# Performance work log

Measured on AMD Instinct MI355X. Metric: run time of the kernel, lower is better.

Reference implementation:

```python
import jax, jax.numpy as jnp
import numpy as np
from jax.scipy.special import erf

B, N, D = 4, 4096, 2
MU, ALPHA, BETA, SIGMA = 1.0, 0.8, 2.0, 0.02


def setup_inputs() -> dict:
    key = jax.random.key(0)
    k1, k2 = jax.random.split(key)
    locations = jax.random.uniform(k1, (B, N, D), dtype=jnp.float32)  # events in unit box
    times = jnp.sort(jax.random.uniform(k2, (B, N), dtype=jnp.float32), axis=-1)  # sorted event times
    # ragged sequence lengths via mask
    lengths = jnp.array([N, N - 256, N - 512, N - 1024], dtype=jnp.int32)
    mask = jnp.arange(N)[None, :] < lengths[:, None]
    return {
        "locations": locations,
        "times": times,
        "mask": mask,
        "mu": jnp.float32(MU),
        "alpha": jnp.float32(ALPHA),
        "beta": jnp.float32(BETA),
        "sigma": jnp.float32(SIGMA),
        "spatial_low": jnp.zeros((D,), jnp.float32),
        "spatial_high": jnp.ones((D,), jnp.float32),
        "t_end": jnp.float32(1.0),
    }


def reference(locations, times, mask, mu, alpha, beta, sigma, spatial_low, spatial_high, t_end):
    """Hawkes log_prob: sum_i log lambda*(s_i, t_i | H_{t_i}) - Lambda(D x [0, T])."""
    d = locations.shape[-1]
    # --- intensity at each event given its (strictly earlier, masked) history ---
    dt = times[:, :, None] - times[:, None, :]            # [B,N,N] t_i - t_j
    valid = (dt > 0.0) & mask[:, None, :]                 # causal + observed history
    dt_safe = jnp.where(valid, dt, 0.0)
    diff = locations[:, :, None, :] - locations[:, None, :, :]  # [B,N,N,D]
    sqdist = jnp.sum(diff * diff, axis=-1)                # [B,N,N]
    two_sig2 = 2.0 * sigma * sigma
    # fused exp of temporal decay * spatial Gaussian exponent
    kern = jnp.where(valid, jnp.exp(-beta * dt_safe - sqdist / two_sig2), 0.0)
    norm = beta / (jnp.pi * two_sig2) ** (d / 2)          # beta * (2*pi*sigma^2)^(-d/2)
    lam = mu + alpha * norm * jnp.sum(kern, axis=-1)      # [B,N]
    log_lam = jnp.sum(jnp.where(mask, jnp.log(lam), 0.0), axis=-1)  # [B]
    # --- compensator with erf boundary correction ---
    s_sqrt2 = sigma * jnp.sqrt(jnp.float32(2.0))
    cdf = 0.5 * (erf((spatial_high - locations) / s_sqrt2)
                 - erf((spatial_low - locations) / s_sqrt2))        # [B,N,D]
    in_domain_mass = jnp.prod(cdf, axis=-1)               # [B,N]
    temporal_mass = 1.0 - jnp.exp(-beta * (t_end - times))  # [B,N]
    area = jnp.prod(spatial_high - spatial_low)
    comp = mu * area * t_end + alpha * jnp.sum(
        jnp.where(mask, temporal_mass * in_domain_mass, 0.0), axis=-1)  # [B]
    return log_lam - comp
```

## Files before the change

kernel.cpp:

```cpp
#include <hip/hip_runtime.h>
#include <math.h>

#define NB   4096
#define BB   4
#define TI   512
#define TJ   128
#define NSL  (NB / TJ)
#define NIT  (NB / TI)
#define THR  256
#define TPB  144

#if __has_builtin(__builtin_amdgcn_exp2f)
#define EXP2F __builtin_amdgcn_exp2f
#else
#define EXP2F exp2f
#endif

__global__ __launch_bounds__(THR) void hawkes_pair(
    const float* __restrict__ loc, const float* __restrict__ times,
    const int* __restrict__ mask,
    const float* __restrict__ beta_p, const float* __restrict__ sigma_p,
    float* __restrict__ S)
{
    const int b  = blockIdx.x / TPB;
    const int k  = blockIdx.x % TPB;
    int it = (int)floorf((sqrtf((float)(2 * k + 1)) - 1.0f) * 0.5f);
    while (2 * (it + 1) * (it + 1) + 2 * (it + 1) <= k) ++it;
    while (2 * it * it + 2 * it > k) --it;
    const int s = k - (2 * it * it + 2 * it);

    const int tid = threadIdx.x;
    const int i0 = it * TI + tid;
    const int i1 = i0 + THR;

    const float beta  = beta_p[0];
    const float sigma = sigma_p[0];
    const float L2E = 1.4426950408889634f;
    const float nb  = -beta * L2E;
    const float nc  = -L2E / (2.0f * sigma * sigma);

    const float t0 = times[b * NB + i0];
    const float x0 = loc[(b * NB + i0) * 2 + 0];
    const float y0 = loc[(b * NB + i0) * 2 + 1];
    const float u0 = fmaf(nc, fmaf(x0, x0, y0 * y0), nb * t0);
    const float t1 = times[b * NB + i1];
    const float x1 = loc[(b * NB + i1) * 2 + 0];
    const float y1 = loc[(b * NB + i1) * 2 + 1];
    const float u1 = fmaf(nc, fmaf(x1, x1, y1 * y1), nb * t1);

    __shared__ float4 jt[TJ];
    if (tid < TJ) {
        const int j  = s * TJ + tid;
        const float tj = times[b * NB + j];
        const float xj = loc[(b * NB + j) * 2 + 0];
        const float yj = loc[(b * NB + j) * 2 + 1];
        const bool  mj = mask[b * NB + j] != 0;
        float4 v;
        v.x = mj ? fmaf(nc, fmaf(xj, xj, yj * yj), -nb * tj) : -3.0e38f;
        v.y = mj ? (-2.0f * nc * xj) : 0.0f;
        v.z = mj ? (-2.0f * nc * yj) : 0.0f;
        v.w = mj ? tj : 2.0f;
        jt[tid] = v;
    }
    __syncthreads();

    float a0 = 0.0f, a1 = 0.0f;
    if (s < 4 * it) {
#pragma unroll 8
        for (int jj = 0; jj < TJ; ++jj) {
            float4 v = jt[jj];
            float g0 = fmaf(v.y, x0, fmaf(v.z, y0, u0 + v.x));
            float g1 = fmaf(v.y, x1, fmaf(v.z, y1, u1 + v.x));
            a0 += EXP2F(g0);
            a1 += EXP2F(g1);
        }
    } else {
#pragma unroll 8
        for (int jj = 0; jj < TJ; ++jj) {
            float4 v = jt[jj];
            float g0 = fmaf(v.y, x0, fmaf(v.z, y0, u0 + v.x));
            float g1 = fmaf(v.y, x1, fmaf(v.z, y1, u1 + v.x));
            float e0 = EXP2F(g0);
            float e1 = EXP2F(g1);
            a0 += (t0 > v.w) ? e0 : 0.0f;
            a1 += (t1 > v.w) ? e1 : 0.0f;
        }
    }
    float* __restrict__ Srow = S + (size_t)(b * NSL + s) * NB;
    Srow[i0] = a0;
    Srow[i1] = a1;
}

__global__ __launch_bounds__(1024) void hawkes_finish(
    const float* __restrict__ loc, const float* __restrict__ times,
    const int* __restrict__ mask,
    const float* mu_p, const float* alpha_p, const float* beta_p, const float* sigma_p,
    const float* lo_p, const float* hi_p, const float* tend_p,
    const float* __restrict__ S, float* __restrict__ out)
{
    const int b   = blockIdx.x;
    const int tid = threadIdx.x;

    const float mu    = mu_p[0];
    const float alpha = alpha_p[0];
    const float beta  = beta_p[0];
    const float sigma = sigma_p[0];
    const float lo0 = lo_p[0], lo1 = lo_p[1];
    const float hi0 = hi_p[0], hi1 = hi_p[1];
    const float tend = tend_p[0];

    const float two_sig2 = 2.0f * sigma * sigma;
    const float an = alpha * beta / ((float)M_PI * two_sig2);
    const float inv_ss2 = 1.0f / (sigma * sqrtf(2.0f));

    float accL = 0.0f, accC = 0.0f;
    for (int i = tid; i < NB; i += 1024) {
        if (mask[b * NB + i] != 0) {
            const int smax = 4 * (i >> 9) + 4;
            float sum = 0.0f;
            for (int s = 0; s < smax; ++s)
                sum += S[(size_t)(b * NSL + s) * NB + i];
            float lam = fmaf(an, sum, mu);
            accL += logf(lam);
            float tmass = 1.0f - expf(-beta * (tend - times[b * NB + i]));
            float x = loc[(b * NB + i) * 2 + 0];
            float y = loc[(b * NB + i) * 2 + 1];
            float cx = 0.5f * (erff((hi0 - x) * inv_ss2) - erff((lo0 - x) * inv_ss2));
            float cy = 0.5f * (erff((hi1 - y) * inv_ss2) - erff((lo1 - y) * inv_ss2));
            accC += tmass * cx * cy;
        }
    }

    __shared__ float redL[16], redC[16];
    for (int off = 32; off > 0; off >>= 1) {
        accL += __shfl_down(accL, off, 64);
        accC += __shfl_down(accC, off, 64);
    }
    const int wave = tid >> 6, lane = tid & 63;
    if (lane == 0) { redL[wave] = accL; redC[wave] = accC; }
    __syncthreads();
    if (tid == 0) {
        float L = 0.0f, C = 0.0f;
#pragma unroll
        for (int w = 0; w < 16; ++w) { L += redL[w]; C += redC[w]; }
        float area = (hi0 - lo0) * (hi1 - lo1);
        out[b] = L - (mu * area * tend + alpha * C);
    }
}

extern "C" void kernel_launch(void* const* d_in, const int* in_sizes, int n_in,
                              void* d_out, int out_size, void* d_ws, size_t ws_size,
                              hipStream_t stream) {
    const float* loc   = (const float*)d_in[0];
    const float* times = (const float*)d_in[1];
    const int*   mask  = (const int*)d_in[2];
    const float* mu_p    = (const float*)d_in[3];
    const float* alpha_p = (const float*)d_in[4];
    const float* beta_p  = (const float*)d_in[5];
    const float* sigma_p = (const float*)d_in[6];
    const float* lo_p    = (const float*)d_in[7];
    const float* hi_p    = (const float*)d_in[8];
    const float* tend_p  = (const float*)d_in[9];
    float* out = (float*)d_out;
    float* S   = (float*)d_ws;

    hawkes_pair<<<dim3(BB * TPB), THR, 0, stream>>>(loc, times, mask, beta_p, sigma_p, S);
    hawkes_finish<<<dim3(BB), 1024, 0, stream>>>(loc, times, mask, mu_p, alpha_p, beta_p,
                                                 sigma_p, lo_p, hi_p, tend_p, S, out);
}
```

Before: 104.6 us.

## Shrink pair tiles and split finish reduction across blocks with atomics

The pair kernel now uses 256-row i-tiles with 128 threads, giving finer triangular tiling and more blocks (272 per batch instead of 144). The finish kernel is spread over 64 blocks of 256 threads instead of 4 blocks of 1024. Partial sums are combined through global atomics, and a completion counter lets the last block write the output. This adds more parallelism to the latency-bound finish stage and trims the diagonal waste in the pair stage, at the cost of atomic traffic and extra workspace used for accumulators.

```diff
diff --git a/kernel.cpp b/kernel.cpp
--- a/kernel.cpp
+++ b/kernel.cpp
@@ -3,18 +3,19 @@
 
 #define NB   4096
 #define BB   4
-#define TI   512
+#define TI   256
 #define TJ   128
 #define NSL  (NB / TJ)
-#define NIT  (NB / TI)
-#define THR  256
-#define TPB  144
+#define THR  128
+#define TPB  272
 
 #if __has_builtin(__builtin_amdgcn_exp2f)
 #define EXP2F __builtin_amdgcn_exp2f
 #else
 #define EXP2F exp2f
 #endif
+
+#define S_ELEMS (BB * NSL * NB)
 
 __global__ __launch_bounds__(THR) void hawkes_pair(
     const float* __restrict__ loc, const float* __restrict__ times,
@@ -24,12 +25,20 @@
 {
     const int b  = blockIdx.x / TPB;
     const int k  = blockIdx.x % TPB;
-    int it = (int)floorf((sqrtf((float)(2 * k + 1)) - 1.0f) * 0.5f);
-    while (2 * (it + 1) * (it + 1) + 2 * (it + 1) <= k) ++it;
-    while (2 * it * it + 2 * it > k) --it;
-    const int s = k - (2 * it * it + 2 * it);
+    int it = (int)floorf((sqrtf((float)(4 * k + 1)) - 1.0f) * 0.5f);
+    while ((it + 1) * (it + 1) + (it + 1) <= k) ++it;
+    while (it * it + it > k) --it;
+    const int s = k - (it * it + it);
 
     const int tid = threadIdx.x;
+
+    if (k == 0 && tid == 0) {
+        float* acc = S + S_ELEMS;
+        acc[b] = 0.0f;
+        acc[BB + b] = 0.0f;
+        ((int*)(acc + 2 * BB))[b] = 0;
+    }
+
     const int i0 = it * TI + tid;
     const int i1 = i0 + THR;
 
@@ -49,7 +58,7 @@
     const float u1 = fmaf(nc, fmaf(x1, x1, y1 * y1), nb * t1);
 
     __shared__ float4 jt[TJ];
-    if (tid < TJ) {
+    {
         const int j  = s * TJ + tid;
         const float tj = times[b * NB + j];
         const float xj = loc[(b * NB + j) * 2 + 0];
@@ -65,7 +74,7 @@
     __syncthreads();
 
     float a0 = 0.0f, a1 = 0.0f;
-    if (s < 4 * it) {
+    if (s < 2 * it) {
 #pragma unroll 8
         for (int jj = 0; jj < TJ; ++jj) {
             float4 v = jt[jj];
@@ -91,15 +100,17 @@
     Srow[i1] = a1;
 }
 
-__global__ __launch_bounds__(1024) void hawkes_finish(
+__global__ __launch_bounds__(256) void hawkes_finish(
     const float* __restrict__ loc, const float* __restrict__ times,
     const int* __restrict__ mask,
     const float* mu_p, const float* alpha_p, const float* beta_p, const float* sigma_p,
     const float* lo_p, const float* hi_p, const float* tend_p,
-    const float* __restrict__ S, float* __restrict__ out)
+    float* __restrict__ S, float* __restrict__ out)
 {
-    const int b   = blockIdx.x;
+    const int b   = blockIdx.x >> 4;
+    const int r   = blockIdx.x & 15;
     const int tid = threadIdx.x;
+    const int i   = r * 256 + tid;
 
     const float mu    = mu_p[0];
     const float alpha = alpha_p[0];
@@ -114,24 +125,22 @@
     const float inv_ss2 = 1.0f / (sigma * sqrtf(2.0f));
 
     float accL = 0.0f, accC = 0.0f;
-    for (int i = tid; i < NB; i += 1024) {
-        if (mask[b * NB + i] != 0) {
-            const int smax = 4 * (i >> 9) + 4;
-            float sum = 0.0f;
-            for (int s = 0; s < smax; ++s)
-                sum += S[(size_t)(b * NSL + s) * NB + i];
-            float lam = fmaf(an, sum, mu);
-            accL += logf(lam);
-            float tmass = 1.0f - expf(-beta * (tend - times[b * NB + i]));
-            float x = loc[(b * NB + i) * 2 + 0];
-            float y = loc[(b * NB + i) * 2 + 1];
-            float cx = 0.5f * (erff((hi0 - x) * inv_ss2) - erff((lo0 - x) * inv_ss2));
-            float cy = 0.5f * (erff((hi1 - y) * inv_ss2) - erff((lo1 - y) * inv_ss2));
-            accC += tmass * cx * cy;
-        }
+    if (mask[b * NB + i] != 0) {
+        const int smax = 2 * (i >> 8) + 2;
+        float sum = 0.0f;
+        for (int s = 0; s < smax; ++s)
+            sum += S[(size_t)(b * NSL + s) * NB + i];
+        float lam = fmaf(an, sum, mu);
+        accL = logf(lam);
+        float tmass = 1.0f - expf(-beta * (tend - times[b * NB + i]));
+        float x = loc[(b * NB + i) * 2 + 0];
+        float y = loc[(b * NB + i) * 2 + 1];
+        float cx = 0.5f * (erff((hi0 - x) * inv_ss2) - erff((lo0 - x) * inv_ss2));
+        float cy = 0.5f * (erff((hi1 - y) * inv_ss2) - erff((lo1 - y) * inv_ss2));
+        accC = tmass * cx * cy;
     }
 
-    __shared__ float redL[16], redC[16];
+    __shared__ float redL[4], redC[4];
     for (int off = 32; off > 0; off >>= 1) {
         accL += __shfl_down(accL, off, 64);
         accC += __shfl_down(accC, off, 64);
@@ -139,12 +148,24 @@
     const int wave = tid >> 6, lane = tid & 63;
     if (lane == 0) { redL[wave] = accL; redC[wave] = accC; }
     __syncthreads();
+
     if (tid == 0) {
-        float L = 0.0f, C = 0.0f;
-#pragma unroll
-        for (int w = 0; w < 16; ++w) { L += redL[w]; C += redC[w]; }
-        float area = (hi0 - lo0) * (hi1 - lo1);
-        out[b] = L - (mu * area * tend + alpha * C);
+        float L = redL[0] + redL[1] + redL[2] + redL[3];
+        float C = redC[0] + redC[1] + redC[2] + redC[3];
+        float* accLg = S + S_ELEMS;
+        float* accCg = accLg + BB;
+        int*   cnt   = (int*)(accLg + 2 * BB);
+        atomicAdd(&accLg[b], L);
+        atomicAdd(&accCg[b], C);
+        __threadfence();
+        int old = atomicAdd(&cnt[b], 1);
+        if (old == 15) {
+            __threadfence();
+            float Lt = atomicAdd(&accLg[b], 0.0f);
+            float Ct = atomicAdd(&accCg[b], 0.0f);
+            float area = (hi0 - lo0) * (hi1 - lo1);
+            out[b] = Lt - (mu * area * tend + alpha * Ct);
+        }
     }
 }
 
@@ -165,6 +186,6 @@
     float* S   = (float*)d_ws;
 
     hawkes_pair<<<dim3(BB * TPB), THR, 0, stream>>>(loc, times, mask, beta_p, sigma_p, S);
-    hawkes_finish<<<dim3(BB), 1024, 0, stream>>>(loc, times, mask, mu_p, alpha_p, beta_p,
-                                                 sigma_p, lo_p, hi_p, tend_p, S, out);
+    hawkes_finish<<<dim3(BB * 16), 256, 0, stream>>>(loc, times, mask, mu_p, alpha_p, beta_p,
+                                                     sigma_p, lo_p, hi_p, tend_p, S, out);
 }
```

Result: faster. 91.24 us (-12.7%).
